# Kernel tuning notes

Measured on AMD Instinct MI355X. Metric: run time of the kernel, lower is better.

## Reference

```python
import jax, jax.numpy as jnp
import numpy as np
from jax import lax

N_NODES = 50000
N_EDGES = 1_600_000
B, T = 4, 12
GCN_H, TCN_H, OUT_LEN = 32, 32, 1


def setup_inputs() -> dict:
    key = jax.random.key(0)
    ks = jax.random.split(key, 8)
    return {
        "x_seq": jax.random.normal(ks[0], (B, T, N_NODES), jnp.float32),
        "edge_index": jax.random.randint(ks[1], (2, N_EDGES), 0, N_NODES, jnp.int64),
        "edge_weight": jax.random.uniform(ks[2], (N_EDGES,), jnp.float32),
        "gcn_w": jax.random.normal(ks[3], (1, GCN_H), jnp.float32) * 0.5,
        "gcn_b": jnp.zeros((GCN_H,), jnp.float32),
        "conv_w": jax.random.normal(ks[4], (TCN_H, GCN_H, 3), jnp.float32) * 0.1,
        "conv_b": jnp.zeros((TCN_H,), jnp.float32),
        "lin_w": jax.random.normal(ks[5], (TCN_H, OUT_LEN), jnp.float32) * 0.1,
        "lin_b": jnp.zeros((OUT_LEN,), jnp.float32),
    }


def _gcn_agg(x, src, dst, norm, n):
    msgs = x[:, src] * norm[None, :]                      # [BT, E+N]
    return jax.vmap(lambda m: jax.ops.segment_sum(m, dst, num_segments=n))(msgs)


def reference(x_seq, edge_index, edge_weight, gcn_w, gcn_b, conv_w, conv_b, lin_w, lin_b):
    b, t, n = x_seq.shape
    src, dst = edge_index[0], edge_index[1]
    # GCN normalization with self-loops (fill_value=1.0), as PyG GCNConv
    loops = jnp.arange(n)
    src_f = jnp.concatenate([src, loops])
    dst_f = jnp.concatenate([dst, loops])
    ew_f = jnp.concatenate([edge_weight, jnp.ones((n,), x_seq.dtype)])
    deg = jax.ops.segment_sum(ew_f, dst_f, num_segments=n)
    dinv = jnp.where(deg > 0, deg ** -0.5, 0.0)
    norm = dinv[src_f] * ew_f * dinv[dst_f]               # [E+N]
    # GCN is linear: A_hat (X W) == (A_hat X) W ; X has 1 channel -> aggregate scalars
    x = x_seq.reshape(b * t, n)                           # [BT, N]
    agg = _gcn_agg(x, src_f, dst_f, norm, n)              # [BT, N]
    h = agg[..., None] * gcn_w[0][None, None, :] + gcn_b  # [BT, N, H]
    # temporal conv over T: reshape to [B*N, H, T]
    h = h.reshape(b, t, n, GCN_H).transpose(0, 2, 3, 1).reshape(b * n, GCN_H, t)
    y = lax.conv_general_dilated(h, conv_w, window_strides=(1,), padding=[(1, 1)],
                                 dimension_numbers=("NCH", "OIH", "NCH"))
    y = jax.nn.relu(y + conv_b[None, :, None])            # [B*N, H, T]
    pooled = y.mean(axis=-1)                              # [B*N, H]
    out = pooled @ lin_w + lin_b                          # [B*N, out_len]
    return out.reshape(b, n, -1).transpose(0, 2, 1)       # [B, out_len, N]
```

## Files before the change

### kernel.cpp

```cpp
#include <hip/hip_runtime.h>
#include <hip/hip_fp16.h>
#include <math.h>

#define N_NODES 50000
#define N_EDGES 1600000
#define BT 48
#define CAP 80
#define BINSZ 64
#define NBINS 782
#define ECHUNK 4096
#define SBLOCK 1024

__global__ __launch_bounds__(SBLOCK) void stage_k(const int* __restrict__ ei,
                                                  const float* __restrict__ ew,
                                                  int* __restrict__ stage_cnt,
                                                  int2* __restrict__ staged,
                                                  int scap) {
  __shared__ int hist[NBINS];
  __shared__ int ptr[NBINS];
  int t = threadIdx.x;
  for (int b = t; b < NBINS; b += SBLOCK) hist[b] = 0;
  __syncthreads();

  int e0 = blockIdx.x * ECHUNK;
  int ne = min(ECHUNK, N_EDGES - e0);

  for (int k = t; k < ne; k += SBLOCK) {
    int d = ei[N_EDGES + e0 + k];
    atomicAdd(&hist[d >> 6], 1);
  }
  __syncthreads();
  for (int b = t; b < NBINS; b += SBLOCK) {
    int h = hist[b];
    ptr[b] = h ? atomicAdd(&stage_cnt[b], h) : 0;
  }
  __syncthreads();
  for (int k = t; k < ne; k += SBLOCK) {
    int e = e0 + k;
    int s = ei[e];
    int d = ei[N_EDGES + e];
    float w = ew[e];
    int b = d >> 6;
    int p = atomicAdd(&ptr[b], 1);
    if (p < scap)
      staged[(size_t)b * scap + p] = make_int2(s | ((d & 63) << 16), __float_as_int(w));
  }
}

__global__ __launch_bounds__(1024) void scan_k(const int* __restrict__ sc,
                                               int* __restrict__ bin_base) {
  __shared__ int buf[1024];
  int t = threadIdx.x;
  int v = (t < NBINS) ? sc[t] : 0;
  buf[t] = v;
  __syncthreads();
  for (int off = 1; off < 1024; off <<= 1) {
    int x = (t >= off) ? buf[t - off] : 0;
    __syncthreads();
    buf[t] += x;
    __syncthreads();
  }
  if (t < NBINS) bin_base[t] = buf[t] - v;
}

__global__ __launch_bounds__(256) void build_k(const int2* __restrict__ staged,
                                               const int* __restrict__ stage_cnt,
                                               const int* __restrict__ bin_base,
                                               int* __restrict__ packed,
                                               int* __restrict__ row_desc,
                                               float* __restrict__ dinv,
                                               int scap) {
  __shared__ int2 rows[BINSZ][CAP];
  __shared__ int rcnt[BINSZ];
  __shared__ int loc[BINSZ + 1];
  int t = threadIdx.x, b = blockIdx.x;
  if (t < BINSZ) rcnt[t] = 0;
  __syncthreads();

  int ne = min(stage_cnt[b], scap);
  const int2* sp = staged + (size_t)b * scap;
  for (int k = t; k < ne; k += 256) {
    int2 m = sp[k];
    int dloc = (m.x >> 16) & 63;
    int src  = m.x & 0xffff;
    int slot = atomicAdd(&rcnt[dloc], 1);
    if (slot < CAP) rows[dloc][slot] = make_int2(src, m.y);
  }
  __syncthreads();

  if (t == 0) {
    int run = 0;
    for (int r = 0; r < BINSZ; ++r) {
      loc[r] = run;
      run += min(rcnt[r], CAP);
    }
    loc[BINSZ] = run;
  }
  __syncthreads();

  int base = b * BINSZ;
  int gbase = bin_base[b];
  if (t < BINSZ) {
    int n = base + t;
    if (n < N_NODES) {
      int c = min(rcnt[t], CAP);
      float s = 0.0f;
      for (int i = 0; i < c; ++i) s += __int_as_float(rows[t][i].y);
      dinv[n] = 1.0f / sqrtf(1.0f + s);
      row_desc[n] = ((gbase + loc[t]) << 7) | c;
    }
  }
  __syncthreads();

  int r = t & 63, st = t >> 6;
  int n = base + r;
  if (n < N_NODES) {
    int c = min(rcnt[r], CAP);
    int* dst = packed + gbase + loc[r];
    for (int i = st; i < c; i += 4) {
      int2 e = rows[r][i];
      unsigned hw = __half_as_ushort(__float2half_rn(__int_as_float(e.y)));
      dst[i] = (e.x & 0xffff) | ((int)hw << 16);
    }
  }
}

__global__ __launch_bounds__(256) void transpose_k(const float* __restrict__ x,
                                                   const float* __restrict__ dinv,
                                                   __half* __restrict__ xs) {
  int n = blockIdx.x * 256 + threadIdx.x;
  if (n >= N_NODES) return;
  float dn = dinv[n];
  __half2 h2[BT / 2];
#pragma unroll
  for (int j = 0; j < BT / 2; ++j) {
    float a = dn * x[(size_t)(2 * j) * N_NODES + n];
    float b = dn * x[(size_t)(2 * j + 1) * N_NODES + n];
    h2[j] = __floats2half2_rn(a, b);
  }
  float4* dst = (float4*)(xs + (size_t)n * BT);
  const float4* srcp = (const float4*)h2;
#pragma unroll
  for (int j = 0; j < 6; ++j) dst[j] = srcp[j];
}

__global__ void coeff_k(const float* __restrict__ conv_w, const float* __restrict__ gcn_w,
                        const float* __restrict__ gcn_b, float* __restrict__ wv,
                        float* __restrict__ wb) {
  int idx = threadIdx.x;
  if (idx >= 96) return;
  int co = idx / 3, k = idx % 3;
  float sv = 0.0f, sb = 0.0f;
  for (int ci = 0; ci < 32; ++ci) {
    float w = conv_w[co * 96 + ci * 3 + k];
    sv += w * gcn_w[ci];
    sb += w * gcn_b[ci];
  }
  wv[idx] = sv;
  wb[idx] = sb;
}

__global__ __launch_bounds__(256) void spmm_epi_k(const __half* __restrict__ xs,
                                                  const int* __restrict__ packed,
                                                  const int* __restrict__ row_desc,
                                                  const float* __restrict__ dinv,
                                                  const float* __restrict__ wv,
                                                  const float* __restrict__ wb,
                                                  const float* __restrict__ conv_b,
                                                  const float* __restrict__ lin_w,
                                                  const float* __restrict__ lin_b,
                                                  float* __restrict__ out) {
  __shared__ float s_wv[96], s_wb[96], s_cb[32], s_lw[32];
  __shared__ float s_lb;
  __shared__ float sAgg[4][BT];
  int tid = threadIdx.x;
  if (tid < 96) { s_wv[tid] = wv[tid]; s_wb[tid] = wb[tid]; }
  if (tid < 32) { s_cb[tid] = conv_b[tid]; s_lw[tid] = lin_w[tid]; }
  if (tid == 0) s_lb = lin_b[0];
  __syncthreads();

  int lane = tid & 63;
  int wid  = tid >> 6;
  int n = (blockIdx.x * 256 + tid) >> 6;
  int col = (lane < BT) ? lane : (BT - 1);
  int desc = __builtin_amdgcn_readfirstlane(row_desc[n]);
  int c     = desc & 127;
  int start = ((unsigned)desc) >> 7;
  const int* pp = packed + start;
  int m = pp[lane];
  float acc = 0.0f;
  int cm = (c < 64) ? c : 64;

  int e = 0;
  for (; e + 16 <= cm; e += 16) {
    float xv[16], wg[16];
#pragma unroll
    for (int k = 0; k < 16; ++k) {
      int u = __builtin_amdgcn_readlane(m, e + k);
      int s = u & 0xffff;
      wg[k] = __half2float(__ushort_as_half((unsigned short)(((unsigned)u) >> 16)));
      xv[k] = __half2float(xs[s * BT + col]);
    }
#pragma unroll
    for (int k = 0; k < 16; ++k) acc = fmaf(wg[k], xv[k], acc);
  }
  for (; e + 8 <= cm; e += 8) {
    float xv[8], wg[8];
#pragma unroll
    for (int k = 0; k < 8; ++k) {
      int u = __builtin_amdgcn_readlane(m, e + k);
      int s = u & 0xffff;
      wg[k] = __half2float(__ushort_as_half((unsigned short)(((unsigned)u) >> 16)));
      xv[k] = __half2float(xs[s * BT + col]);
    }
#pragma unroll
    for (int k = 0; k < 8; ++k) acc = fmaf(wg[k], xv[k], acc);
  }
  for (; e < cm; ++e) {
    int u = __builtin_amdgcn_readlane(m, e);
    int s = u & 0xffff;
    float w = __half2float(__ushort_as_half((unsigned short)(((unsigned)u) >> 16)));
    acc = fmaf(w, __half2float(xs[s * BT + col]), acc);
  }
  for (; e < c; ++e) {
    int u = __builtin_amdgcn_readfirstlane(pp[e]);
    int s = u & 0xffff;
    float w = __half2float(__ushort_as_half((unsigned short)(((unsigned)u) >> 16)));
    acc = fmaf(w, __half2float(xs[s * BT + col]), acc);
  }

  float dn = dinv[n];
  float xsn = __half2float(xs[n * BT + col]);
  if (lane < BT) sAgg[wid][col] = dn * (acc + xsn);

  int b = lane >> 4;
  float a[14];
  a[0] = 0.0f; a[13] = 0.0f;
#pragma unroll
  for (int t = 0; t < 12; ++t) a[t + 1] = sAgg[wid][b * 12 + t];

  float part = 0.0f;
#pragma unroll
  for (int cc = 0; cc < 2; ++cc) {
    int co = (lane & 15) + cc * 16;
    float w0 = s_wv[3 * co], w1 = s_wv[3 * co + 1], w2 = s_wv[3 * co + 2];
    float b0 = s_wb[3 * co], b1 = s_wb[3 * co + 1], b2 = s_wb[3 * co + 2];
    float base = s_cb[co] + b1;
    float lw = s_lw[co];
    float sr = 0.0f;
#pragma unroll
    for (int t = 0; t < 12; ++t) {
      float v = base + w0 * a[t] + w1 * a[t + 1] + w2 * a[t + 2];
      if (t > 0)  v += b0;
      if (t < 11) v += b2;
      sr += fmaxf(v, 0.0f);
    }
    part = fmaf(lw, sr, part);
  }
  part += __shfl_xor(part, 1, 64);
  part += __shfl_xor(part, 2, 64);
  part += __shfl_xor(part, 4, 64);
  part += __shfl_xor(part, 8, 64);
  if ((lane & 15) == 0)
    out[(size_t)b * N_NODES + n] = s_lb + part * (1.0f / 12.0f);
}

extern "C" void kernel_launch(void* const* d_in, const int* in_sizes, int n_in,
                              void* d_out, int out_size, void* d_ws, size_t ws_size,
                              hipStream_t stream) {
  const float* x_seq  = (const float*)d_in[0];
  const int*   ei     = (const int*)d_in[1];
  const float* ew     = (const float*)d_in[2];
  const float* gcn_w  = (const float*)d_in[3];
  const float* gcn_b  = (const float*)d_in[4];
  const float* conv_w = (const float*)d_in[5];
  const float* conv_b = (const float*)d_in[6];
  const float* lin_w  = (const float*)d_in[7];
  const float* lin_b  = (const float*)d_in[8];
  float* out = (float*)d_out;

  char* ws = (char*)d_ws;
  size_t off = 0;
  auto alloc = [&](size_t bytes) -> void* {
    void* p = ws + off;
    off += (bytes + 511) & ~(size_t)511;
    return p;
  };
  float* dinv    = (float*)alloc((size_t)N_NODES * 4);
  int*   rdesc   = (int*)alloc((size_t)N_NODES * 4);
  float* wv      = (float*)alloc(96 * 4);
  float* wb      = (float*)alloc(96 * 4);
  int*   sc      = (int*)alloc((size_t)NBINS * 4);
  int*   bbase   = (int*)alloc((size_t)NBINS * 4);
  int*   packed  = (int*)alloc(((size_t)N_EDGES + 64) * 4);

  size_t remain = (ws_size > off) ? (ws_size - off) : 0;
  int scap = (int)(remain / ((size_t)NBINS * 8));
  if (scap > 4096) scap = 4096;
  if (scap < 3072) scap = 3072;
  int2* staged = (int2*)alloc((size_t)NBINS * scap * 8);
  __half* xs = (__half*)staged;

  const int nblk = (N_NODES + 255) / 256;
  const int sblk = (N_EDGES + ECHUNK - 1) / ECHUNK;
  const int wblk = (N_NODES * 64) / 256;

  hipMemsetAsync(sc, 0, (size_t)NBINS * 4, stream);
  hipLaunchKernelGGL(stage_k, dim3(sblk), dim3(SBLOCK), 0, stream, ei, ew, sc, staged, scap);
  hipLaunchKernelGGL(scan_k, dim3(1), dim3(1024), 0, stream, sc, bbase);
  hipLaunchKernelGGL(build_k, dim3(NBINS), dim3(256), 0, stream,
                     staged, sc, bbase, packed, rdesc, dinv, scap);
  hipLaunchKernelGGL(transpose_k, dim3(nblk), dim3(256), 0, stream, x_seq, dinv, xs);
  hipLaunchKernelGGL(coeff_k, dim3(1), dim3(128), 0, stream, conv_w, gcn_w, gcn_b, wv, wb);
  hipLaunchKernelGGL(spmm_epi_k, dim3(wblk), dim3(256), 0, stream,
                     xs, packed, rdesc, dinv, wv, wb, conv_b, lin_w, lin_b, out);
}
```

Baseline: 190.4 us.

## Sort edges locally per chunk and gather with 4-edge lane groups in SpMM

Edge binning becomes a two-level scheme. Each chunk sorts its edges by destination bin in shared memory and writes per-chunk histograms and offsets, which replaces the global atomic counters and the fixed-capacity staging area. The build kernel then gathers each bin's segments from every chunk. In the SpMM, node features are padded to 64 half columns so each lane group loads 4 columns per edge with int2 loads and processes 4 edges in parallel via bpermute, followed by a cross-group shuffle reduction. The intent is to remove global atomic contention and scalar per-edge serialization, at the cost of more per-chunk metadata and scattered small reads in build_k.

```diff
diff --git a/kernel.cpp b/kernel.cpp
--- a/kernel.cpp
+++ b/kernel.cpp
@@ -5,57 +5,73 @@
 #define N_NODES 50000
 #define N_EDGES 1600000
 #define BT 48
+#define XCOLS 64
 #define CAP 80
 #define BINSZ 64
 #define NBINS 782
 #define ECHUNK 4096
-#define SBLOCK 1024
-
-__global__ __launch_bounds__(SBLOCK) void stage_k(const int* __restrict__ ei,
-                                                  const float* __restrict__ ew,
-                                                  int* __restrict__ stage_cnt,
-                                                  int2* __restrict__ staged,
-                                                  int scap) {
-  __shared__ int hist[NBINS];
-  __shared__ int ptr[NBINS];
+#define NCHUNK 391
+
+__global__ __launch_bounds__(1024) void stage_k(const int* __restrict__ ei,
+                                                const float* __restrict__ ew,
+                                                int2* __restrict__ staged,
+                                                int* __restrict__ H,
+                                                int* __restrict__ O) {
+  __shared__ int2 sbuf[ECHUNK];
+  __shared__ int hist[NBINS], off[NBINS], ptr[NBINS];
   int t = threadIdx.x;
-  for (int b = t; b < NBINS; b += SBLOCK) hist[b] = 0;
+  if (t < NBINS) hist[t] = 0;
   __syncthreads();
 
   int e0 = blockIdx.x * ECHUNK;
   int ne = min(ECHUNK, N_EDGES - e0);
 
-  for (int k = t; k < ne; k += SBLOCK) {
-    int d = ei[N_EDGES + e0 + k];
-    atomicAdd(&hist[d >> 6], 1);
-  }
-  __syncthreads();
-  for (int b = t; b < NBINS; b += SBLOCK) {
-    int h = hist[b];
-    ptr[b] = h ? atomicAdd(&stage_cnt[b], h) : 0;
-  }
-  __syncthreads();
-  for (int k = t; k < ne; k += SBLOCK) {
+  for (int k = t; k < ne; k += 1024)
+    atomicAdd(&hist[ei[N_EDGES + e0 + k] >> 6], 1);
+  __syncthreads();
+
+  int* buf = (int*)sbuf;
+  int v = (t < NBINS) ? hist[t] : 0;
+  buf[t] = v;
+  __syncthreads();
+  for (int o = 1; o < 1024; o <<= 1) {
+    int x = (t >= o) ? buf[t - o] : 0;
+    __syncthreads();
+    buf[t] += x;
+    __syncthreads();
+  }
+  if (t < NBINS) { off[t] = buf[t] - v; ptr[t] = 0; }
+  __syncthreads();
+
+  for (int k = t; k < ne; k += 1024) {
     int e = e0 + k;
-    int s = ei[e];
-    int d = ei[N_EDGES + e];
+    int s = ei[e], d = ei[N_EDGES + e];
     float w = ew[e];
     int b = d >> 6;
-    int p = atomicAdd(&ptr[b], 1);
-    if (p < scap)
-      staged[(size_t)b * scap + p] = make_int2(s | ((d & 63) << 16), __float_as_int(w));
-  }
-}
-
-__global__ __launch_bounds__(1024) void scan_k(const int* __restrict__ sc,
+    int p = off[b] + atomicAdd(&ptr[b], 1);
+    sbuf[p] = make_int2(s | ((d & 63) << 16), __float_as_int(w));
+  }
+  __syncthreads();
+
+  int2* dst = staged + (size_t)blockIdx.x * ECHUNK;
+  for (int k = t; k < ne; k += 1024) dst[k] = sbuf[k];
+  if (t < NBINS) {
+    H[blockIdx.x * NBINS + t] = hist[t];
+    O[blockIdx.x * NBINS + t] = off[t];
+  }
+}
+
+__global__ __launch_bounds__(1024) void scan_k(const int* __restrict__ H,
                                                int* __restrict__ bin_base) {
   __shared__ int buf[1024];
   int t = threadIdx.x;
-  int v = (t < NBINS) ? sc[t] : 0;
+  int v = 0;
+  if (t < NBINS)
+    for (int c = 0; c < NCHUNK; ++c) v += H[c * NBINS + t];
   buf[t] = v;
   __syncthreads();
-  for (int off = 1; off < 1024; off <<= 1) {
-    int x = (t >= off) ? buf[t - off] : 0;
+  for (int o = 1; o < 1024; o <<= 1) {
+    int x = (t >= o) ? buf[t - o] : 0;
     __syncthreads();
     buf[t] += x;
     __syncthreads();
@@ -64,36 +80,40 @@
 }
 
 __global__ __launch_bounds__(256) void build_k(const int2* __restrict__ staged,
-                                               const int* __restrict__ stage_cnt,
+                                               const int* __restrict__ H,
+                                               const int* __restrict__ O,
                                                const int* __restrict__ bin_base,
                                                int* __restrict__ packed,
                                                int* __restrict__ row_desc,
-                                               float* __restrict__ dinv,
-                                               int scap) {
+                                               float* __restrict__ dinv) {
   __shared__ int2 rows[BINSZ][CAP];
   __shared__ int rcnt[BINSZ];
   __shared__ int loc[BINSZ + 1];
+  __shared__ int cH[NCHUNK], cO[NCHUNK];
   int t = threadIdx.x, b = blockIdx.x;
   if (t < BINSZ) rcnt[t] = 0;
-  __syncthreads();
-
-  int ne = min(stage_cnt[b], scap);
-  const int2* sp = staged + (size_t)b * scap;
-  for (int k = t; k < ne; k += 256) {
-    int2 m = sp[k];
-    int dloc = (m.x >> 16) & 63;
-    int src  = m.x & 0xffff;
-    int slot = atomicAdd(&rcnt[dloc], 1);
-    if (slot < CAP) rows[dloc][slot] = make_int2(src, m.y);
+  for (int c = t; c < NCHUNK; c += 256) {
+    cH[c] = H[c * NBINS + b];
+    cO[c] = O[c * NBINS + b];
+  }
+  __syncthreads();
+
+  int grp = t >> 3, sub8 = t & 7;
+  for (int c = grp; c < NCHUNK; c += 32) {
+    int cnt = cH[c];
+    const int2* src = staged + (size_t)c * ECHUNK + cO[c];
+    for (int k = sub8; k < cnt; k += 8) {
+      int2 m = src[k];
+      int dloc = (m.x >> 16) & 63;
+      int slot = atomicAdd(&rcnt[dloc], 1);
+      if (slot < CAP) rows[dloc][slot] = m;
+    }
   }
   __syncthreads();
 
   if (t == 0) {
     int run = 0;
-    for (int r = 0; r < BINSZ; ++r) {
-      loc[r] = run;
-      run += min(rcnt[r], CAP);
-    }
+    for (int r = 0; r < BINSZ; ++r) { loc[r] = run; run += min(rcnt[r], CAP); }
     loc[BINSZ] = run;
   }
   __syncthreads();
@@ -131,17 +151,19 @@
   int n = blockIdx.x * 256 + threadIdx.x;
   if (n >= N_NODES) return;
   float dn = dinv[n];
-  __half2 h2[BT / 2];
+  __half2 h2[XCOLS / 2];
 #pragma unroll
   for (int j = 0; j < BT / 2; ++j) {
     float a = dn * x[(size_t)(2 * j) * N_NODES + n];
     float b = dn * x[(size_t)(2 * j + 1) * N_NODES + n];
     h2[j] = __floats2half2_rn(a, b);
   }
-  float4* dst = (float4*)(xs + (size_t)n * BT);
-  const float4* srcp = (const float4*)h2;
-#pragma unroll
-  for (int j = 0; j < 6; ++j) dst[j] = srcp[j];
+#pragma unroll
+  for (int j = BT / 2; j < XCOLS / 2; ++j) h2[j] = __floats2half2_rn(0.0f, 0.0f);
+  float4* dst = (float4*)(xs + (size_t)n * XCOLS);
+  const float4* s4 = (const float4*)h2;
+#pragma unroll
+  for (int j = 0; j < 8; ++j) dst[j] = s4[j];
 }
 
 __global__ void coeff_k(const float* __restrict__ conv_w, const float* __restrict__ gcn_w,
@@ -159,6 +181,20 @@
   wv[idx] = sv;
   wb[idx] = sb;
 }
+
+#define PROC(mreg, ebase, MASKED, cs)                                                   \
+  {                                                                                     \
+    int u = __builtin_amdgcn_ds_bpermute(((ebase) << 2) + g4, (mreg));                  \
+    float wf = __half2float(__ushort_as_half((unsigned short)(((unsigned)u) >> 16)));   \
+    if (MASKED) wf = (((ebase) + gi) < (cs)) ? wf : 0.0f;                               \
+    int2 lv = xrow[(u & 0xffff) * (XCOLS / 4) + sub];                                   \
+    __half2 h0 = *reinterpret_cast<__half2*>(&lv.x);                                    \
+    __half2 h1 = *reinterpret_cast<__half2*>(&lv.y);                                    \
+    a0 = fmaf(wf, __half2float(__low2half(h0)), a0);                                    \
+    a1 = fmaf(wf, __half2float(__high2half(h0)), a1);                                   \
+    a2 = fmaf(wf, __half2float(__low2half(h1)), a2);                                    \
+    a3 = fmaf(wf, __half2float(__high2half(h1)), a3);                                   \
+  }
 
 __global__ __launch_bounds__(256) void spmm_epi_k(const __half* __restrict__ xs,
                                                   const int* __restrict__ packed,
@@ -182,56 +218,46 @@
   int lane = tid & 63;
   int wid  = tid >> 6;
   int n = (blockIdx.x * 256 + tid) >> 6;
-  int col = (lane < BT) ? lane : (BT - 1);
+  int gi = lane >> 4, g4 = gi << 2, sub = lane & 15;
+  const int2* xrow = (const int2*)xs;
+
   int desc = __builtin_amdgcn_readfirstlane(row_desc[n]);
   int c     = desc & 127;
   int start = ((unsigned)desc) >> 7;
   const int* pp = packed + start;
-  int m = pp[lane];
-  float acc = 0.0f;
-  int cm = (c < 64) ? c : 64;
+  int m1 = pp[lane];
+  float a0 = 0.f, a1 = 0.f, a2 = 0.f, a3 = 0.f;
+  int c1 = (c < 64) ? c : 64;
 
   int e = 0;
-  for (; e + 16 <= cm; e += 16) {
-    float xv[16], wg[16];
-#pragma unroll
-    for (int k = 0; k < 16; ++k) {
-      int u = __builtin_amdgcn_readlane(m, e + k);
-      int s = u & 0xffff;
-      wg[k] = __half2float(__ushort_as_half((unsigned short)(((unsigned)u) >> 16)));
-      xv[k] = __half2float(xs[s * BT + col]);
-    }
-#pragma unroll
-    for (int k = 0; k < 16; ++k) acc = fmaf(wg[k], xv[k], acc);
-  }
-  for (; e + 8 <= cm; e += 8) {
-    float xv[8], wg[8];
-#pragma unroll
-    for (int k = 0; k < 8; ++k) {
-      int u = __builtin_amdgcn_readlane(m, e + k);
-      int s = u & 0xffff;
-      wg[k] = __half2float(__ushort_as_half((unsigned short)(((unsigned)u) >> 16)));
-      xv[k] = __half2float(xs[s * BT + col]);
-    }
-#pragma unroll
-    for (int k = 0; k < 8; ++k) acc = fmaf(wg[k], xv[k], acc);
-  }
-  for (; e < cm; ++e) {
-    int u = __builtin_amdgcn_readlane(m, e);
-    int s = u & 0xffff;
-    float w = __half2float(__ushort_as_half((unsigned short)(((unsigned)u) >> 16)));
-    acc = fmaf(w, __half2float(xs[s * BT + col]), acc);
-  }
-  for (; e < c; ++e) {
-    int u = __builtin_amdgcn_readfirstlane(pp[e]);
-    int s = u & 0xffff;
-    float w = __half2float(__ushort_as_half((unsigned short)(((unsigned)u) >> 16)));
-    acc = fmaf(w, __half2float(xs[s * BT + col]), acc);
-  }
+  for (; e + 16 <= c1; e += 16) {
+    PROC(m1, e + 0,  false, 0)
+    PROC(m1, e + 4,  false, 0)
+    PROC(m1, e + 8,  false, 0)
+    PROC(m1, e + 12, false, 0)
+  }
+  for (; e < c1; e += 4) PROC(m1, e, true, c1)
+  if (c > 64) {
+    int m2 = pp[64 + lane];
+    int c2 = c - 64;
+    for (int e2 = 0; e2 < c2; e2 += 4) PROC(m2, e2, true, c2)
+  }
+
+  a0 += __shfl_xor(a0, 16, 64); a0 += __shfl_xor(a0, 32, 64);
+  a1 += __shfl_xor(a1, 16, 64); a1 += __shfl_xor(a1, 32, 64);
+  a2 += __shfl_xor(a2, 16, 64); a2 += __shfl_xor(a2, 32, 64);
+  a3 += __shfl_xor(a3, 16, 64); a3 += __shfl_xor(a3, 32, 64);
 
   float dn = dinv[n];
-  float xsn = __half2float(xs[n * BT + col]);
-  if (lane < BT) sAgg[wid][col] = dn * (acc + xsn);
+  if (lane < 12) {
+    int2 lv = xrow[n * (XCOLS / 4) + lane];
+    __half2 h0 = *reinterpret_cast<__half2*>(&lv.x);
+    __half2 h1 = *reinterpret_cast<__half2*>(&lv.y);
+    sAgg[wid][lane * 4 + 0] = dn * (a0 + __half2float(__low2half(h0)));
+    sAgg[wid][lane * 4 + 1] = dn * (a1 + __half2float(__high2half(h0)));
+    sAgg[wid][lane * 4 + 2] = dn * (a2 + __half2float(__low2half(h1)));
+    sAgg[wid][lane * 4 + 3] = dn * (a3 + __half2float(__high2half(h1)));
+  }
 
   int b = lane >> 4;
   float a[14];
@@ -290,26 +316,20 @@
   int*   rdesc   = (int*)alloc((size_t)N_NODES * 4);
   float* wv      = (float*)alloc(96 * 4);
   float* wb      = (float*)alloc(96 * 4);
-  int*   sc      = (int*)alloc((size_t)NBINS * 4);
-  int*   bbase   = (int*)alloc((size_t)NBINS * 4);
-  int*   packed  = (int*)alloc(((size_t)N_EDGES + 64) * 4);
-
-  size_t remain = (ws_size > off) ? (ws_size - off) : 0;
-  int scap = (int)(remain / ((size_t)NBINS * 8));
-  if (scap > 4096) scap = 4096;
-  if (scap < 3072) scap = 3072;
-  int2* staged = (int2*)alloc((size_t)NBINS * scap * 8);
+  int*   H       = (int*)alloc((size_t)NCHUNK * NBINS * 4);
+  int*   Ofs     = (int*)alloc((size_t)NCHUNK * NBINS * 4);
+  int*   bbase   = (int*)alloc(1024 * 4);
+  int*   packed  = (int*)alloc(((size_t)N_EDGES + 192) * 4);
+  int2*  staged  = (int2*)alloc((size_t)NCHUNK * ECHUNK * 8);
   __half* xs = (__half*)staged;
 
   const int nblk = (N_NODES + 255) / 256;
-  const int sblk = (N_EDGES + ECHUNK - 1) / ECHUNK;
   const int wblk = (N_NODES * 64) / 256;
 
-  hipMemsetAsync(sc, 0, (size_t)NBINS * 4, stream);
-  hipLaunchKernelGGL(stage_k, dim3(sblk), dim3(SBLOCK), 0, stream, ei, ew, sc, staged, scap);
-  hipLaunchKernelGGL(scan_k, dim3(1), dim3(1024), 0, stream, sc, bbase);
+  hipLaunchKernelGGL(stage_k, dim3(NCHUNK), dim3(1024), 0, stream, ei, ew, staged, H, Ofs);
+  hipLaunchKernelGGL(scan_k, dim3(1), dim3(1024), 0, stream, H, bbase);
   hipLaunchKernelGGL(build_k, dim3(NBINS), dim3(256), 0, stream,
-                     staged, sc, bbase, packed, rdesc, dinv, scap);
+                     staged, H, Ofs, bbase, packed, rdesc, dinv);
   hipLaunchKernelGGL(transpose_k, dim3(nblk), dim3(256), 0, stream, x_seq, dinv, xs);
   hipLaunchKernelGGL(coeff_k, dim3(1), dim3(128), 0, stream, conv_w, gcn_w, gcn_b, wv, wb);
   hipLaunchKernelGGL(spmm_epi_k, dim3(wblk), dim3(256), 0, stream,
```

Result: slower. 199.9 us (+5.0%).
